# Kernel tuning notes

Measured on AMD Instinct MI355X. Metric: run time of the kernel, lower is better.

Reference implementation:

```python
import jax, jax.numpy as jnp
import numpy as np

B, T, C = 4, 2048, 1024
H, D = 16, 64  # num_heads, head_size


def setup_inputs() -> dict:
    key = jax.random.key(0)
    ks = jax.random.split(key, 5)
    s = 0.02
    x = jax.random.normal(ks[0], (B, T, C), dtype=jnp.float32)
    Wq = jax.random.normal(ks[1], (H, C, D), dtype=jnp.float32) * s
    Wk = jax.random.normal(ks[2], (H, C, D), dtype=jnp.float32) * s
    Wv = jax.random.normal(ks[3], (H, C, D), dtype=jnp.float32) * s
    Wp = jax.random.normal(ks[4], (C, H * D), dtype=jnp.float32) * s  # Linear(H*D, C) weight
    bp = jnp.zeros((C,), dtype=jnp.float32)
    return {"x": x, "Wq": Wq, "Wk": Wk, "Wv": Wv, "Wp": Wp, "bp": bp}


def reference(x, Wq, Wk, Wv, Wp, bp):
    # per-head projections (all heads batched): [B,T,C] x [H,C,D] -> [B,H,T,D]
    q = jnp.einsum('btc,hcd->bhtd', x, Wq)
    k = jnp.einsum('btc,hcd->bhtd', x, Wk)
    v = jnp.einsum('btc,hcd->bhtd', x, Wv)
    scale = 1.0 / jnp.sqrt(jnp.asarray(D, dtype=x.dtype))
    scores = jnp.einsum('bhtd,bhsd->bhts', q, k) * scale  # [B,H,T,T]
    causal = jnp.tril(jnp.ones((T, T), dtype=bool))
    scores = jnp.where(causal, scores, -jnp.inf)
    w = jax.nn.softmax(scores, axis=-1)
    out = jnp.einsum('bhts,bhsd->bhtd', w, v)  # [B,H,T,D]
    out = out.transpose(0, 2, 1, 3).reshape(B, T, H * D)  # concat heads
    return out @ Wp.T + bp  # projection (dropout is identity in eval)
```

## Files before the change

kernel.cpp:

```cpp
#include <hip/hip_runtime.h>
#include <stdint.h>


typedef unsigned short u16;
typedef __attribute__((ext_vector_type(8))) short    s16x8;
typedef __attribute__((ext_vector_type(4))) float    f32x4;
typedef __attribute__((ext_vector_type(2))) uint32_t u32x2;


__device__ __forceinline__ u16 f2b(float f) {
  union { float f; uint32_t u; } v; v.f = f;
  uint32_t r = v.u + 0x7FFFu + ((v.u >> 16) & 1u);
  return (u16)(r >> 16);
}

__device__ __forceinline__ uint32_t cvtpk(float a, float b) {
  uint32_t r;
  asm("v_cvt_pk_bf16_f32 %0, %1, %2" : "=v"(r) : "v"(a), "v"(b));
  return r;
}

__device__ __forceinline__ f32x4 mfma_bf16(s16x8 a, s16x8 b, f32x4 c) {
  asm("v_mfma_f32_16x16x32_bf16 %0, %1, %2, %0" : "+v"(c) : "v"(a), "v"(b));
  return c;
}

__device__ __forceinline__ void gload_lds16(const void* g, void* l) {
  __builtin_amdgcn_global_load_lds(
      (__attribute__((address_space(1))) void*)(uintptr_t)g,
      (__attribute__((address_space(3))) void*)(uint32_t)(uintptr_t)l,
      16, 0, 0);
}


__global__ void cvt_f32_bf16_kernel(const float* __restrict__ in, u16* __restrict__ out) {
  size_t i = (size_t)blockIdx.x * 256 + threadIdx.x;
  const f32x4* p = (const f32x4*)(in + i * 8);
  f32x4 a = p[0], b = p[1];
  s16x8 o;
  o[0]=(short)f2b(a[0]); o[1]=(short)f2b(a[1]); o[2]=(short)f2b(a[2]); o[3]=(short)f2b(a[3]);
  o[4]=(short)f2b(b[0]); o[5]=(short)f2b(b[1]); o[6]=(short)f2b(b[2]); o[7]=(short)f2b(b[3]);
  *(s16x8*)(out + i * 8) = o;
}

__global__ void cvt_wqkv_kernel(const float* __restrict__ Wq, const float* __restrict__ Wk,
                                const float* __restrict__ Wv, u16* __restrict__ out) {
  int idx = blockIdx.x * 256 + threadIdx.x;
  int sel = idx >> 20;
  int rem = idx & 1048575;
  int n = rem >> 10, c = rem & 1023;
  int h = n >> 6, d = n & 63;
  const float* W = (sel == 0) ? Wq : ((sel == 1) ? Wk : Wv);
  out[idx] = f2b(W[h * 65536 + c * 64 + d]);
}


template <int MODE>
__global__ __launch_bounds__(256) void gemm_bt_kernel(
    const u16* __restrict__ A, const u16* __restrict__ B, void* __restrict__ Cout,
    const float* __restrict__ bias, u16* __restrict__ vTout, int K, int ldc)
{
  __shared__ __attribute__((aligned(16))) u16 As[128 * 64];
  __shared__ __attribute__((aligned(16))) u16 Bs[128 * 64];

  const int tid  = threadIdx.x;
  const int lane = tid & 63;
  const int w    = tid >> 6;
  const int wm   = w >> 1, wn = w & 1;
  const int g    = lane >> 4;
  const int li   = lane & 15;
  const size_t bm = (size_t)blockIdx.x * 128;
  const size_t bn = (size_t)blockIdx.y * 128;

  f32x4 acc[4][4] = {};

  const int kIters = K >> 6;
  for (int kt = 0; kt < kIters; ++kt) {
    const int kb = kt * 64;
#pragma unroll
    for (int i = 0; i < 4; ++i) {
      int c = i * 256 + tid;
      int row = c >> 3, sl = c & 7;
      int ss = sl ^ (row & 7);
      gload_lds16(A + (bm + row) * K + kb + ss * 8, &As[c * 8]);
      gload_lds16(B + (bn + row) * K + kb + ss * 8, &Bs[c * 8]);
    }
    __syncthreads();
#pragma unroll
    for (int ks = 0; ks < 2; ++ks) {
      s16x8 af[4], bfr[4];
#pragma unroll
      for (int f = 0; f < 4; ++f) {
        int ra = wm * 64 + f * 16 + li;
        int sa = (ks * 4 + g) ^ (ra & 7);
        af[f] = *(const s16x8*)&As[ra * 64 + sa * 8];
        int rb = wn * 64 + f * 16 + li;
        int sb = (ks * 4 + g) ^ (rb & 7);
        bfr[f] = *(const s16x8*)&Bs[rb * 64 + sb * 8];
      }
#pragma unroll
      for (int mi = 0; mi < 4; ++mi)
#pragma unroll
        for (int ni = 0; ni < 4; ++ni)
          acc[mi][ni] = mfma_bf16(af[mi], bfr[ni], acc[mi][ni]);
    }
    __syncthreads();
  }

  if constexpr (MODE == 1) {
#pragma unroll
    for (int ni = 0; ni < 4; ++ni) {
      size_t col = bn + wn * 64 + ni * 16 + li;
      float bv = bias[col];
#pragma unroll
      for (int mi = 0; mi < 4; ++mi)
#pragma unroll
        for (int r = 0; r < 4; ++r) {
          size_t row = bm + wm * 64 + mi * 16 + g * 4 + r;
          ((float*)Cout)[row * ldc + col] = acc[mi][ni][r] + bv;
        }
    }
  } else {
    if (bn < 2048) {
#pragma unroll
      for (int ni = 0; ni < 4; ++ni) {
        size_t col = bn + wn * 64 + ni * 16 + li;
#pragma unroll
        for (int mi = 0; mi < 4; ++mi)
#pragma unroll
          for (int r = 0; r < 4; ++r) {
            size_t row = bm + wm * 64 + mi * 16 + g * 4 + r;
            ((u16*)Cout)[row * ldc + col] = f2b(acc[mi][ni][r]);
          }
      }
    } else {
      const int hb = (int)((bn - 2048) >> 6) + wn;
      const int bb = (int)(bm >> 11);
      const int t0b = ((int)bm & 2047) + wm * 64 + g * 4;
      u16* vrow = vTout + (size_t)((bb * 16 + hb) * 64) * 2048;
#pragma unroll
      for (int ni = 0; ni < 4; ++ni) {
        u16* vd_ = vrow + (size_t)(ni * 16 + li) * 2048;
#pragma unroll
        for (int mi = 0; mi < 4; ++mi) {
          u32x2 wv = { cvtpk(acc[mi][ni][0], acc[mi][ni][1]),
                       cvtpk(acc[mi][ni][2], acc[mi][ni][3]) };
          *(u32x2*)&vd_[t0b + mi * 16] = wv;
        }
      }
    }
  }
}


__global__ __launch_bounds__(256, 4) void attn_kernel(const u16* __restrict__ qkv,
                                                      const u16* __restrict__ vT,
                                                      u16* __restrict__ out) {
  __shared__ __attribute__((aligned(16))) u16 Ks[2][64 * 64];
  __shared__ __attribute__((aligned(16))) u16 Vs[2][64 * 64];
  __shared__ __attribute__((aligned(16))) u16 Ps[4][16 * 64];

  const int id  = blockIdx.x;
  const int xcd = id & 7;
  const int rr  = id >> 3;
  const int bh  = xcd * 8 + (rr & 7);
  const int p   = rr >> 3;

  const int b = bh >> 4, h = bh & 15;
  const int tid = threadIdx.x;
  const int lane = tid & 63;
  const int w = tid >> 6;
  const int g = lane >> 4, li = lane & 15;

  const int tA = 31 - p;
  const int nA = tA + 1;
  const int nTot = nA + p + 1;

  const u16* kbase = qkv + (size_t)(b * 2048) * 3072 + 1024 + h * 64;
  const u16* vtb   = vT + (size_t)bh * 64 * 2048;
  u16* pl = Ps[w];

  const int srow = tid >> 3;
  const int ssl0 = (tid & 7) ^ (srow & 7);
  const int kge0 = srow * 3072 + ssl0 * 8;
  const int vge0 = srow * 2048 + ssl0 * 8;
  u16* const kd0 = &Ks[0][tid * 8];
  u16* const vd0 = &Vs[0][tid * 8];

  int foff[2][4];
#pragma unroll
  for (int kk = 0; kk < 2; ++kk)
#pragma unroll
    for (int fj = 0; fj < 4; ++fj) {
      int rk = fj * 16 + li;
      foff[kk][fj] = rk * 64 + (((kk * 4 + g) ^ (rk & 7)) * 8);
    }
  const int lsw = li & 14;
  int pwoff[4], proff[2];
#pragma unroll
  for (int fj = 0; fj < 4; ++fj) pwoff[fj] = li * 64 + (((4 * fj + g) ^ lsw) * 4);
#pragma unroll
  for (int kk = 0; kk < 2; ++kk) proff[kk] = li * 64 + (((8 * kk + 2 * g) ^ lsw) * 4);

  auto stage = [&](int buf, int j0) {
    const u16* kp = kbase + (size_t)j0 * 3072;
    const u16* vp = vtb + j0;
    u16* kd = kd0 + buf * 4096;
    u16* vd = vd0 + buf * 4096;
    gload_lds16(kp + kge0, kd);
    gload_lds16(kp + kge0 + 32 * 3072, kd + 2048);
    gload_lds16(vp + vge0, vd);
    gload_lds16(vp + vge0 + 32 * 2048, vd + 2048);
  };

  stage(0, 0);
  __syncthreads();

  s16x8 qf[2];
  f32x4 oacc[4];
  float mrow = -1e30f, lrow = 0.f;
  int qglob = 0;
  const float cexp = 0.18033688011112042f;

  for (int s = 0; s < nTot; ++s) {
    const int cur = s & 1;
    const bool inA = s < nA;
    const int t  = inA ? s : s - nA;
    const int qt = inA ? tA : p;
    const int j0 = t * 64;

    if (s + 1 < nTot) {
      int t1 = (s + 1 < nA) ? (s + 1) : (s + 1 - nA);
      stage(cur ^ 1, t1 * 64);
    }

    if (t == 0) {
      qglob = qt * 64 + w * 16 + li;
      const u16* qbase = qkv + (size_t)(b * 2048 + qglob) * 3072 + h * 64;
#pragma unroll
      for (int kk = 0; kk < 2; ++kk)
        qf[kk] = *(const s16x8*)&qbase[kk * 32 + g * 8];
      mrow = -1e30f; lrow = 0.f;
#pragma unroll
      for (int fd = 0; fd < 4; ++fd) oacc[fd] = (f32x4)0.f;
    }

    const u16* ksb = &Ks[0][0] + cur * 4096;
    const u16* vsb = &Vs[0][0] + cur * 4096;

    f32x4 sfr[4] = {};
    __builtin_amdgcn_s_setprio(1);
#pragma unroll
    for (int kk = 0; kk < 2; ++kk) {
      s16x8 kf[4];
#pragma unroll
      for (int fj = 0; fj < 4; ++fj) kf[fj] = *(const s16x8*)&ksb[foff[kk][fj]];
#pragma unroll
      for (int fj = 0; fj < 4; ++fj) sfr[fj] = mfma_bf16(kf[fj], qf[kk], sfr[fj]);
    }
    __builtin_amdgcn_s_setprio(0);

    if (t == qt) {
#pragma unroll
      for (int fj = 0; fj < 4; ++fj)
#pragma unroll
        for (int r = 0; r < 4; ++r) {
          int jj = j0 + fj * 16 + g * 4 + r;
          if (jj > qglob) sfr[fj][r] = -1e30f;
        }
    }

    float mx = sfr[0][0];
#pragma unroll
    for (int fj = 0; fj < 4; ++fj)
#pragma unroll
      for (int r = 0; r < 4; ++r) mx = fmaxf(mx, sfr[fj][r]);
    mx = fmaxf(mx, __shfl_xor(mx, 16));
    mx = fmaxf(mx, __shfl_xor(mx, 32));

    bool need = (mx - mrow) * cexp > 8.0f;
    if (__any(need)) {
      float mnew = fmaxf(mrow, mx);
      float sc = exp2f((mrow - mnew) * cexp);
      mrow = mnew;
      lrow *= sc;
#pragma unroll
      for (int fd = 0; fd < 4; ++fd)
#pragma unroll
        for (int r = 0; r < 4; ++r) oacc[fd][r] *= sc;
    }

    float rs = 0.f;
#pragma unroll
    for (int fj = 0; fj < 4; ++fj) {
      float p0 = exp2f((sfr[fj][0] - mrow) * cexp);
      float p1 = exp2f((sfr[fj][1] - mrow) * cexp);
      float p2 = exp2f((sfr[fj][2] - mrow) * cexp);
      float p3 = exp2f((sfr[fj][3] - mrow) * cexp);
      rs += (p0 + p1) + (p2 + p3);
      u32x2 wv = { cvtpk(p0, p1), cvtpk(p2, p3) };
      *(u32x2*)&pl[pwoff[fj]] = wv;
    }
    rs += __shfl_xor(rs, 16);
    rs += __shfl_xor(rs, 32);
    lrow += rs;

    __builtin_amdgcn_s_setprio(1);
#pragma unroll
    for (int kk = 0; kk < 2; ++kk) {
      s16x8 pf = *(const s16x8*)&pl[proff[kk]];
      s16x8 vf[4];
#pragma unroll
      for (int fd = 0; fd < 4; ++fd) vf[fd] = *(const s16x8*)&vsb[foff[kk][fd]];
#pragma unroll
      for (int fd = 0; fd < 4; ++fd) oacc[fd] = mfma_bf16(vf[fd], pf, oacc[fd]);
    }
    __builtin_amdgcn_s_setprio(0);

    if (t == qt) {
      float inv = 1.f / lrow;
      u16* ob = out + (size_t)(b * 2048 + qglob) * 1024 + h * 64;
#pragma unroll
      for (int fd = 0; fd < 4; ++fd) {
        u32x2 wv = { cvtpk(oacc[fd][0] * inv, oacc[fd][1] * inv),
                     cvtpk(oacc[fd][2] * inv, oacc[fd][3] * inv) };
        *(u32x2*)&ob[fd * 16 + g * 4] = wv;
      }
    }

    __syncthreads();
  }
}


extern "C" void kernel_launch(void* const* d_in, const int* in_sizes, int n_in,
                              void* d_out, int out_size, void* d_ws, size_t ws_size,
                              hipStream_t stream) {
  const float* x  = (const float*)d_in[0];
  const float* Wq = (const float*)d_in[1];
  const float* Wk = (const float*)d_in[2];
  const float* Wv = (const float*)d_in[3];
  const float* Wp = (const float*)d_in[4];
  const float* bp = (const float*)d_in[5];
  (void)in_sizes; (void)n_in; (void)out_size; (void)ws_size;

  char* ws = (char*)d_ws;
  u16* xb    = (u16*)(ws);
  u16* wqkvb = (u16*)(ws + 16777216);
  u16* wpb   = (u16*)(ws + 23068672);
  u16* qkv   = (u16*)(ws + 25165824);
  u16* vT    = (u16*)(ws + 75497472);
  u16* ao    = (u16*)(ws + 92274688);

  cvt_f32_bf16_kernel<<<4096, 256, 0, stream>>>(x, xb);
  cvt_wqkv_kernel<<<12288, 256, 0, stream>>>(Wq, Wk, Wv, wqkvb);
  cvt_f32_bf16_kernel<<<512, 256, 0, stream>>>(Wp, wpb);

  gemm_bt_kernel<2><<<dim3(64, 24), 256, 0, stream>>>(
      xb, wqkvb, (void*)qkv, nullptr, vT, 1024, 3072);

  attn_kernel<<<1024, 256, 0, stream>>>(qkv, vT, ao);

  gemm_bt_kernel<1><<<dim3(64, 8), 256, 0, stream>>>(
      ao, wpb, d_out, bp, nullptr, 1024, 1024);
}
```

Baseline: 175.7 us.

## Widen attention query tile to 128 rows per block with two subtiles per wave

Each attention block now handles a 128-row query tile: each wave computes two 16-row query subtiles against the same K/V tiles, so every staged K/V tile and LDS fragment load is reused twice. The grid drops from 1024 to 512 blocks with paired query tiles (15-p and p), each running 34 steps. The row-sum cross-lane reduction moves to the final output step, and the max reduction only happens when a rescale is needed. Register pressure rises, launch bounds drop to 2 blocks per SM, and the P buffer doubles. Waves whose rows are fully masked skip the tile compute, which can leave waves idle on diagonal tiles.

```diff
diff --git a/kernel.cpp b/kernel.cpp
--- a/kernel.cpp
+++ b/kernel.cpp
@@ -153,12 +153,12 @@
 }
 
 
-__global__ __launch_bounds__(256, 4) void attn_kernel(const u16* __restrict__ qkv,
+__global__ __launch_bounds__(256, 2) void attn_kernel(const u16* __restrict__ qkv,
                                                       const u16* __restrict__ vT,
                                                       u16* __restrict__ out) {
   __shared__ __attribute__((aligned(16))) u16 Ks[2][64 * 64];
   __shared__ __attribute__((aligned(16))) u16 Vs[2][64 * 64];
-  __shared__ __attribute__((aligned(16))) u16 Ps[4][16 * 64];
+  __shared__ __attribute__((aligned(16))) u16 Ps[4][32 * 64];
 
   const int id  = blockIdx.x;
   const int xcd = id & 7;
@@ -172,9 +172,9 @@
   const int w = tid >> 6;
   const int g = lane >> 4, li = lane & 15;
 
-  const int tA = 31 - p;
-  const int nA = tA + 1;
-  const int nTot = nA + p + 1;
+  const int tA  = 15 - p;
+  const int nAi = 2 * (tA + 1);
+  const int nTot = 34;
 
   const u16* kbase = qkv + (size_t)(b * 2048) * 3072 + 1024 + h * 64;
   const u16* vtb   = vT + (size_t)bh * 64 * 2048;
@@ -196,11 +196,16 @@
       foff[kk][fj] = rk * 64 + (((kk * 4 + g) ^ (rk & 7)) * 8);
     }
   const int lsw = li & 14;
-  int pwoff[4], proff[2];
-#pragma unroll
-  for (int fj = 0; fj < 4; ++fj) pwoff[fj] = li * 64 + (((4 * fj + g) ^ lsw) * 4);
-#pragma unroll
-  for (int kk = 0; kk < 2; ++kk) proff[kk] = li * 64 + (((8 * kk + 2 * g) ^ lsw) * 4);
+  int pwoff[2][4], proff[2][2];
+#pragma unroll
+  for (int u = 0; u < 2; ++u) {
+#pragma unroll
+    for (int fj = 0; fj < 4; ++fj)
+      pwoff[u][fj] = (u * 16 + li) * 64 + (((4 * fj + g) ^ lsw) * 4);
+#pragma unroll
+    for (int kk = 0; kk < 2; ++kk)
+      proff[u][kk] = (u * 16 + li) * 64 + (((8 * kk + 2 * g) ^ lsw) * 4);
+  }
 
   auto stage = [&](int buf, int j0) {
     const u16* kp = kbase + (size_t)j0 * 3072;
@@ -216,115 +221,147 @@
   stage(0, 0);
   __syncthreads();
 
-  s16x8 qf[2];
-  f32x4 oacc[4];
-  float mrow = -1e30f, lrow = 0.f;
-  int qglob = 0;
+  s16x8 qf[2][2];
+  f32x4 oacc[2][4];
+  float mrow[2], lrowp[2];
+  int wq0 = 0, qg[2];
   const float cexp = 0.18033688011112042f;
+  const float thr = 8.0f;
 
   for (int s = 0; s < nTot; ++s) {
     const int cur = s & 1;
-    const bool inA = s < nA;
-    const int t  = inA ? s : s - nA;
+    const bool inA = s < nAi;
+    const int t  = inA ? s : s - nAi;
     const int qt = inA ? tA : p;
     const int j0 = t * 64;
+    const int tLast = inA ? (nAi - 1) : (nTot - nAi - 1);
 
     if (s + 1 < nTot) {
-      int t1 = (s + 1 < nA) ? (s + 1) : (s + 1 - nA);
+      int t1 = (s + 1 < nAi) ? (s + 1) : (s + 1 - nAi);
       stage(cur ^ 1, t1 * 64);
     }
 
     if (t == 0) {
-      qglob = qt * 64 + w * 16 + li;
-      const u16* qbase = qkv + (size_t)(b * 2048 + qglob) * 3072 + h * 64;
-#pragma unroll
-      for (int kk = 0; kk < 2; ++kk)
-        qf[kk] = *(const s16x8*)&qbase[kk * 32 + g * 8];
-      mrow = -1e30f; lrow = 0.f;
-#pragma unroll
-      for (int fd = 0; fd < 4; ++fd) oacc[fd] = (f32x4)0.f;
-    }
-
-    const u16* ksb = &Ks[0][0] + cur * 4096;
-    const u16* vsb = &Vs[0][0] + cur * 4096;
-
-    f32x4 sfr[4] = {};
-    __builtin_amdgcn_s_setprio(1);
-#pragma unroll
-    for (int kk = 0; kk < 2; ++kk) {
-      s16x8 kf[4];
-#pragma unroll
-      for (int fj = 0; fj < 4; ++fj) kf[fj] = *(const s16x8*)&ksb[foff[kk][fj]];
-#pragma unroll
-      for (int fj = 0; fj < 4; ++fj) sfr[fj] = mfma_bf16(kf[fj], qf[kk], sfr[fj]);
-    }
-    __builtin_amdgcn_s_setprio(0);
-
-    if (t == qt) {
-#pragma unroll
-      for (int fj = 0; fj < 4; ++fj)
-#pragma unroll
-        for (int r = 0; r < 4; ++r) {
-          int jj = j0 + fj * 16 + g * 4 + r;
-          if (jj > qglob) sfr[fj][r] = -1e30f;
-        }
-    }
-
-    float mx = sfr[0][0];
-#pragma unroll
-    for (int fj = 0; fj < 4; ++fj)
-#pragma unroll
-      for (int r = 0; r < 4; ++r) mx = fmaxf(mx, sfr[fj][r]);
-    mx = fmaxf(mx, __shfl_xor(mx, 16));
-    mx = fmaxf(mx, __shfl_xor(mx, 32));
-
-    bool need = (mx - mrow) * cexp > 8.0f;
-    if (__any(need)) {
-      float mnew = fmaxf(mrow, mx);
-      float sc = exp2f((mrow - mnew) * cexp);
-      mrow = mnew;
-      lrow *= sc;
-#pragma unroll
-      for (int fd = 0; fd < 4; ++fd)
-#pragma unroll
-        for (int r = 0; r < 4; ++r) oacc[fd][r] *= sc;
-    }
-
-    float rs = 0.f;
-#pragma unroll
-    for (int fj = 0; fj < 4; ++fj) {
-      float p0 = exp2f((sfr[fj][0] - mrow) * cexp);
-      float p1 = exp2f((sfr[fj][1] - mrow) * cexp);
-      float p2 = exp2f((sfr[fj][2] - mrow) * cexp);
-      float p3 = exp2f((sfr[fj][3] - mrow) * cexp);
-      rs += (p0 + p1) + (p2 + p3);
-      u32x2 wv = { cvtpk(p0, p1), cvtpk(p2, p3) };
-      *(u32x2*)&pl[pwoff[fj]] = wv;
-    }
-    rs += __shfl_xor(rs, 16);
-    rs += __shfl_xor(rs, 32);
-    lrow += rs;
-
-    __builtin_amdgcn_s_setprio(1);
-#pragma unroll
-    for (int kk = 0; kk < 2; ++kk) {
-      s16x8 pf = *(const s16x8*)&pl[proff[kk]];
-      s16x8 vf[4];
-#pragma unroll
-      for (int fd = 0; fd < 4; ++fd) vf[fd] = *(const s16x8*)&vsb[foff[kk][fd]];
-#pragma unroll
-      for (int fd = 0; fd < 4; ++fd) oacc[fd] = mfma_bf16(vf[fd], pf, oacc[fd]);
-    }
-    __builtin_amdgcn_s_setprio(0);
-
-    if (t == qt) {
-      float inv = 1.f / lrow;
-      u16* ob = out + (size_t)(b * 2048 + qglob) * 1024 + h * 64;
-#pragma unroll
-      for (int fd = 0; fd < 4; ++fd) {
-        u32x2 wv = { cvtpk(oacc[fd][0] * inv, oacc[fd][1] * inv),
-                     cvtpk(oacc[fd][2] * inv, oacc[fd][3] * inv) };
-        *(u32x2*)&ob[fd * 16 + g * 4] = wv;
+      wq0 = qt * 128 + w * 32;
+#pragma unroll
+      for (int u = 0; u < 2; ++u) {
+        qg[u] = wq0 + u * 16 + li;
+        const u16* qbase = qkv + (size_t)(b * 2048 + qg[u]) * 3072 + h * 64;
+#pragma unroll
+        for (int kk = 0; kk < 2; ++kk)
+          qf[u][kk] = *(const s16x8*)&qbase[kk * 32 + g * 8];
+        mrow[u] = -1e30f; lrowp[u] = 0.f;
+#pragma unroll
+        for (int fd = 0; fd < 4; ++fd) oacc[u][fd] = (f32x4)0.f;
+      }
+    }
+
+    if (j0 < wq0 + 32) {
+      const u16* ksb = &Ks[0][0] + cur * 4096;
+      const u16* vsb = &Vs[0][0] + cur * 4096;
+
+      f32x4 sfr[2][4] = {};
+      __builtin_amdgcn_s_setprio(1);
+#pragma unroll
+      for (int kk = 0; kk < 2; ++kk) {
+        s16x8 kf[4];
+#pragma unroll
+        for (int fj = 0; fj < 4; ++fj) kf[fj] = *(const s16x8*)&ksb[foff[kk][fj]];
+#pragma unroll
+        for (int u = 0; u < 2; ++u)
+#pragma unroll
+          for (int fj = 0; fj < 4; ++fj)
+            sfr[u][fj] = mfma_bf16(kf[fj], qf[u][kk], sfr[u][fj]);
+      }
+      __builtin_amdgcn_s_setprio(0);
+
+      if (j0 + 63 > wq0) {
+#pragma unroll
+        for (int u = 0; u < 2; ++u)
+#pragma unroll
+          for (int fj = 0; fj < 4; ++fj)
+#pragma unroll
+            for (int r = 0; r < 4; ++r) {
+              int jj = j0 + fj * 16 + g * 4 + r;
+              if (jj > qg[u]) sfr[u][fj][r] = -1e30f;
+            }
+      }
+
+      float mx[2];
+#pragma unroll
+      for (int u = 0; u < 2; ++u) {
+        float m0 = sfr[u][0][0];
+#pragma unroll
+        for (int fj = 0; fj < 4; ++fj)
+#pragma unroll
+          for (int r = 0; r < 4; ++r) m0 = fmaxf(m0, sfr[u][fj][r]);
+        mx[u] = m0;
+      }
+      bool need = ((mx[0] - mrow[0]) * cexp > thr) | ((mx[1] - mrow[1]) * cexp > thr);
+      if (__any(need)) {
+#pragma unroll
+        for (int u = 0; u < 2; ++u) {
+          float m0 = mx[u];
+          m0 = fmaxf(m0, __shfl_xor(m0, 16));
+          m0 = fmaxf(m0, __shfl_xor(m0, 32));
+          float mnew = fmaxf(mrow[u], m0);
+          float sc = exp2f((mrow[u] - mnew) * cexp);
+          mrow[u] = mnew;
+          lrowp[u] *= sc;
+#pragma unroll
+          for (int fd = 0; fd < 4; ++fd)
+#pragma unroll
+            for (int r = 0; r < 4; ++r) oacc[u][fd][r] *= sc;
+        }
+      }
+
+#pragma unroll
+      for (int u = 0; u < 2; ++u) {
+        float rs = 0.f;
+#pragma unroll
+        for (int fj = 0; fj < 4; ++fj) {
+          float p0 = exp2f((sfr[u][fj][0] - mrow[u]) * cexp);
+          float p1 = exp2f((sfr[u][fj][1] - mrow[u]) * cexp);
+          float p2 = exp2f((sfr[u][fj][2] - mrow[u]) * cexp);
+          float p3 = exp2f((sfr[u][fj][3] - mrow[u]) * cexp);
+          rs += (p0 + p1) + (p2 + p3);
+          u32x2 wv = { cvtpk(p0, p1), cvtpk(p2, p3) };
+          *(u32x2*)&pl[pwoff[u][fj]] = wv;
+        }
+        lrowp[u] += rs;
+      }
+
+      __builtin_amdgcn_s_setprio(1);
+#pragma unroll
+      for (int kk = 0; kk < 2; ++kk) {
+        s16x8 vf[4];
+#pragma unroll
+        for (int fd = 0; fd < 4; ++fd) vf[fd] = *(const s16x8*)&vsb[foff[kk][fd]];
+#pragma unroll
+        for (int u = 0; u < 2; ++u) {
+          s16x8 pf = *(const s16x8*)&pl[proff[u][kk]];
+#pragma unroll
+          for (int fd = 0; fd < 4; ++fd)
+            oacc[u][fd] = mfma_bf16(vf[fd], pf, oacc[u][fd]);
+        }
+      }
+      __builtin_amdgcn_s_setprio(0);
+    }
+
+    if (t == tLast) {
+#pragma unroll
+      for (int u = 0; u < 2; ++u) {
+        float lr = lrowp[u];
+        lr += __shfl_xor(lr, 16);
+        lr += __shfl_xor(lr, 32);
+        float inv = 1.f / lr;
+        u16* ob = out + (size_t)(b * 2048 + qg[u]) * 1024 + h * 64;
+#pragma unroll
+        for (int fd = 0; fd < 4; ++fd) {
+          u32x2 wv = { cvtpk(oacc[u][fd][0] * inv, oacc[u][fd][1] * inv),
+                       cvtpk(oacc[u][fd][2] * inv, oacc[u][fd][3] * inv) };
+          *(u32x2*)&ob[fd * 16 + g * 4] = wv;
+        }
       }
     }
 
@@ -359,7 +396,7 @@
   gemm_bt_kernel<2><<<dim3(64, 24), 256, 0, stream>>>(
       xb, wqkvb, (void*)qkv, nullptr, vT, 1024, 3072);
 
-  attn_kernel<<<1024, 256, 0, stream>>>(qkv, vT, ao);
+  attn_kernel<<<512, 256, 0, stream>>>(qkv, vT, ao);
 
   gemm_bt_kernel<1><<<dim3(64, 8), 256, 0, stream>>>(
       ao, wpb, d_out, bp, nullptr, 1024, 1024);
```

Measured after the change: 174.7 us. Within noise of the previous version (-0.6%).
